# Performance work log

Measured on AMD Instinct MI355X. Metric: run time of the kernel, lower is better.

The kernel has to match this reference:

```python
import jax, jax.numpy as jnp
import numpy as np
from jax import lax

B, T, IN, D, K = 32, 4096, 12, 256, 1024
DECAY = 0.99
EPS_BN = 1e-5
EPS_VQ = 1e-5


def conv1d(x, w, b, pad):
    # x: (B, C, T), w: (O, I, k)
    y = lax.conv_general_dilated(x, w, window_strides=(1,), padding=[(pad, pad)],
                                 dimension_numbers=("NCH", "OIH", "NCH"))
    return y + b[None, :, None]


def batchnorm(x, g, be):
    # training-mode BatchNorm1d: stats over (B, T) per channel, biased variance
    m = jnp.mean(x, axis=(0, 2), keepdims=True)
    v = jnp.mean((x - m) ** 2, axis=(0, 2), keepdims=True)
    return (x - m) * lax.rsqrt(v + EPS_BN) * g[None, :, None] + be[None, :, None]


def setup_inputs() -> dict:
    key = jax.random.key(0)
    ks = jax.random.split(key, 16)
    inp = {"x": jax.random.normal(ks[0], (B, T, IN), dtype=jnp.float32)}
    fan_in = [IN] + [D] * 5
    for i in range(6):
        std = 1.0 / np.sqrt(fan_in[i] * 4)
        inp[f"w{i+1}"] = jax.random.normal(ks[1 + i], (D, fan_in[i], 4), dtype=jnp.float32) * std
        inp[f"b{i+1}"] = jnp.zeros((D,), dtype=jnp.float32)
    for i in range(5):
        inp[f"g{i+1}"] = jnp.ones((D,), dtype=jnp.float32)
        inp[f"be{i+1}"] = jnp.zeros((D,), dtype=jnp.float32)
    inp["codebook"] = jax.random.normal(ks[8], (K, D), dtype=jnp.float32)
    inp["ema_w"] = jax.random.normal(ks[9], (K, D), dtype=jnp.float32)
    inp["ema_cluster_size"] = jnp.zeros((K,), dtype=jnp.float32)
    return inp


def reference(x, w1, b1, g1, be1, w2, b2, g2, be2, w3, b3, g3, be3,
              w4, b4, g4, be4, w5, b5, g5, be5, w6, b6,
              codebook, ema_w, ema_cluster_size):
    h = jnp.transpose(x, (0, 2, 1))  # (B, IN, T)
    h = jax.nn.relu(batchnorm(conv1d(h, w1, b1, 2), g1, be1))
    h = jax.nn.relu(batchnorm(conv1d(h, w2, b2, 1), g2, be2))
    h = jax.nn.relu(batchnorm(conv1d(h, w3, b3, 2), g3, be3))
    h = jax.nn.relu(batchnorm(conv1d(h, w4, b4, 1), g4, be4))
    h = jax.nn.relu(batchnorm(conv1d(h, w5, b5, 2), g5, be5))
    h = conv1d(h, w6, b6, 1)
    z_e = jnp.transpose(h, (0, 2, 1))  # (B, T, D)

    # cdist(p=2) + argmin; sqrt is monotone so argmin over squared dist is identical
    d2 = (jnp.sum(z_e ** 2, axis=-1, keepdims=True)
          - 2.0 * jnp.einsum("btd,kd->btk", z_e, codebook)
          + jnp.sum(codebook ** 2, axis=-1))  # (B, T, K)
    ids = jnp.argmin(d2, axis=-1)  # (B, T)
    z_q = codebook[ids]  # (B, T, D)

    ids_flat = ids.reshape(-1)
    z_e_flat = z_e.reshape(-1, D)
    # one-hot.T @ z_e == segment_sum; one-hot column sums == counts
    n_i = jax.ops.segment_sum(jnp.ones_like(ids_flat, dtype=z_e.dtype), ids_flat, num_segments=K)
    sum_current = jax.ops.segment_sum(z_e_flat, ids_flat, num_segments=K)  # (K, D)

    new_ecs = ema_cluster_size * DECAY + (1.0 - DECAY) * n_i
    n = jnp.sum(new_ecs)
    smoothed = (new_ecs + EPS_VQ) / (n + K * EPS_VQ) * n
    new_ema_w = ema_w * DECAY + (1.0 - DECAY) * sum_current
    new_codebook = new_ema_w / smoothed[:, None]

    z_q_st = z_e + lax.stop_gradient(z_q - z_e)  # straight-through
    return z_e, z_q_st, new_codebook, new_ecs
```

## Files before the change

### kernel.cpp

```cpp
#include <hip/hip_runtime.h>
#include <cstdint>
#include <cstddef>


typedef _Float16 half8 __attribute__((ext_vector_type(8)));
typedef float f32x4 __attribute__((ext_vector_type(4)));

#define MFMA16(a, b, c) __builtin_amdgcn_mfma_f32_16x16x32_f16((a), (b), (c), 0, 0, 0)
#define INV2048 4.8828125e-4f

__device__ __forceinline__ void splitf(float v, _Float16& h, _Float16& l)
{
    _Float16 hh = (_Float16)v;
    h = hh;
    l = (_Float16)((v - (float)hh) * 2048.0f);
}
__device__ __forceinline__ float joinf(_Float16 h, _Float16 l)
{
    return (float)h + (float)l * INV2048;
}

__global__ __launch_bounds__(256)
void conv1_kernel(const float* __restrict__ x, const float* __restrict__ w1,
                  const float* __restrict__ b1, _Float16* __restrict__ YH,
                  _Float16* __restrict__ YL)
{
    const int b  = blockIdx.y;
    const int t0 = blockIdx.x * 32;
    const int oc = threadIdx.x;
    __shared__ float xl[35 * 12];
    for (int idx = threadIdx.x; idx < 420; idx += 256) {
        int tt = t0 - 2 + idx / 12;
        int i  = idx % 12;
        xl[idx] = (tt >= 0 && tt < 4096) ? x[((size_t)b * 4096 + tt) * 12 + i] : 0.f;
    }
    float w[48];
#pragma unroll
    for (int q = 0; q < 12; q++)
        *(float4*)&w[q * 4] = *(const float4*)(w1 + (size_t)oc * 48 + q * 4);
    __syncthreads();
    const float bias = b1[oc];
    for (int dt = 0; dt < 32; dt++) {
        int t = t0 + dt;
        if (t >= 4097) break;
        float a = bias;
#pragma unroll
        for (int i = 0; i < 12; i++)
#pragma unroll
            for (int k = 0; k < 4; k++)
                a = fmaf(xl[(dt + k) * 12 + i], w[i * 4 + k], a);
        _Float16 h, l;
        splitf(a, h, l);
        const size_t o = ((size_t)b * 4097 + t) * 256 + oc;
        YH[o] = h;
        YL[o] = l;
    }
}

__global__ __launch_bounds__(256)
void bn_partial_h(const _Float16* __restrict__ YH, const _Float16* __restrict__ YL,
                  int M, float* __restrict__ part)
{
    const int j = blockIdx.x;
    const int c = threadIdx.x;
    const int chunk = (M + 255) / 256;
    int r0 = j * chunk;
    int r1 = r0 + chunk; if (r1 > M) r1 = M;
    float s = 0.f, s2 = 0.f;
    for (int r = r0; r < r1; r++) {
        const size_t o = ((size_t)r << 8) + c;
        float v = joinf(YH[o], YL[o]);
        s += v;
        s2 = fmaf(v, v, s2);
    }
    part[j * 256 + c]         = s;
    part[65536 + j * 256 + c] = s2;
}

__global__ __launch_bounds__(256)
void bn_finalize(const float* __restrict__ part, const float* __restrict__ g,
                 const float* __restrict__ be, float invM, float* __restrict__ scsh)
{
    const int c = threadIdx.x;
    float s = 0.f, s2 = 0.f;
    for (int j = 0; j < 256; j++) {
        s  += part[j * 256 + c];
        s2 += part[65536 + j * 256 + c];
    }
    float mean = s * invM;
    float var  = fmaf(s2, invM, -mean * mean);
    float sc   = g[c] * rsqrtf(var + 1e-5f);
    scsh[c]       = sc;
    scsh[256 + c] = fmaf(-mean, sc, be[c]);
}

__global__ __launch_bounds__(256)
void bn_split_h(_Float16* __restrict__ YH, _Float16* __restrict__ YL,
                const float* __restrict__ scsh, int N8)
{
    int idx = blockIdx.x * 256 + threadIdx.x;
    const int stride = gridDim.x * 256;
    for (; idx < N8; idx += stride) {
        const size_t e0 = (size_t)idx * 8;
        const int ci0 = (int)(e0 & 255);
        half8 h = *(half8*)(YH + e0);
        half8 l = *(half8*)(YL + e0);
        float4 scA = *(const float4*)(scsh + ci0);
        float4 scB = *(const float4*)(scsh + ci0 + 4);
        float4 shA = *(const float4*)(scsh + 256 + ci0);
        float4 shB = *(const float4*)(scsh + 256 + ci0 + 4);
        float sc[8] = {scA.x, scA.y, scA.z, scA.w, scB.x, scB.y, scB.z, scB.w};
        float sh[8] = {shA.x, shA.y, shA.z, shA.w, shB.x, shB.y, shB.z, shB.w};
#pragma unroll
        for (int e = 0; e < 8; e++) {
            float v = joinf(h[e], l[e]);
            v = fmaxf(fmaf(v, sc[e], sh[e]), 0.f);
            _Float16 hh, ll;
            splitf(v, hh, ll);
            h[e] = hh;
            l[e] = ll;
        }
        *(half8*)(YH + e0) = h;
        *(half8*)(YL + e0) = l;
    }
}

__global__ __launch_bounds__(256)
void split8(const float* __restrict__ Z, _Float16* __restrict__ ZH,
            _Float16* __restrict__ ZL, int N8)
{
    int idx = blockIdx.x * 256 + threadIdx.x;
    const int stride = gridDim.x * 256;
    for (; idx < N8; idx += stride) {
        const size_t e0 = (size_t)idx * 8;
        float4 a = *(const float4*)(Z + e0);
        float4 b = *(const float4*)(Z + e0 + 4);
        float v[8] = {a.x, a.y, a.z, a.w, b.x, b.y, b.z, b.w};
        half8 h, l;
#pragma unroll
        for (int e = 0; e < 8; e++) {
            _Float16 hh, ll;
            splitf(v[e], hh, ll);
            h[e] = hh;
            l[e] = ll;
        }
        *(half8*)(ZH + e0) = h;
        *(half8*)(ZL + e0) = l;
    }
}

__global__ __launch_bounds__(256)
void prep_w_split(const float* __restrict__ w, _Float16* __restrict__ hi,
                  _Float16* __restrict__ lo)
{
    int idx = blockIdx.x * 256 + threadIdx.x;
    int o   = idx >> 10, rem = idx & 1023;
    int tap = rem >> 8,  ci  = rem & 255;
    float v = w[((size_t)o << 10) + (ci << 2) + tap];
    _Float16 h, l;
    splitf(v, h, l);
    hi[idx] = h;
    lo[idx] = l;
}

__global__ __launch_bounds__(256)
void prep_cnorm(const float* __restrict__ cb, float* __restrict__ cnorm)
{
    const int k = blockIdx.x;
    const int d = threadIdx.x;
    float v = cb[((size_t)k << 8) + d];
    __shared__ float sm[256];
    sm[d] = v * v;
    __syncthreads();
    for (int off = 128; off > 0; off >>= 1) {
        if (d < off) sm[d] += sm[d + off];
        __syncthreads();
    }
    if (d == 0) cnorm[k] = sm[0];
}

template<int T_IN, int T_OUT, int PAD, bool F32OUT>
__global__ __launch_bounds__(256)
void conv_gemm_mfma(const _Float16* __restrict__ XH, const _Float16* __restrict__ XL,
                    const _Float16* __restrict__ WH, const _Float16* __restrict__ WL,
                    const float* __restrict__ bias, float* __restrict__ Yf,
                    _Float16* __restrict__ YH, _Float16* __restrict__ YL)
{
    constexpr int M = 32 * T_OUT;
    __shared__ _Float16 AsH[4096], AsL[4096], BsH[4096], BsL[4096];

    const int tid  = threadIdx.x;
    const int lane = tid & 63;
    const int wv   = tid >> 6;
    const int fr   = lane & 15;
    const int kgf  = lane >> 4;
    const int m0 = blockIdx.y * 128;
    const int n0 = blockIdx.x * 128;

    const int haBase = wv * 1024 + ((fr * 32 + kgf * 8) ^ ((fr & 7) << 3));
    const int hbBase = (fr * 32 + kgf * 8) ^ ((fr & 7) << 3);

    const int skg = tid & 3;
    int wOff[2], tOut[2];
    long long aBase[2];
    size_t bBase[2];
    bool mok[2];
#pragma unroll
    for (int u = 0; u < 2; u++) {
        int r = (tid >> 2) + 64 * u;
        wOff[u] = (r * 32 + skg * 8) ^ ((r & 7) << 3);
        int m = m0 + r;
        mok[u] = (m < M);
        int b;
        if (T_OUT == 4096) b = m >> 12;
        else               b = (m - (m >> 12)) >> 12;
        int t = m - b * T_OUT;
        tOut[u]  = t;
        aBase[u] = (((long long)b * T_IN + t) << 8) + (skg << 3);
        bBase[u] = (((size_t)(n0 + r)) << 10) + (skg << 3);
    }

    half8 rAH[2], rAL[2], rBH[2], rBL[2];
    const half8 hz = {(_Float16)0, (_Float16)0, (_Float16)0, (_Float16)0,
                      (_Float16)0, (_Float16)0, (_Float16)0, (_Float16)0};

    auto LOAD = [&](int s) {
        const int tap = s >> 3;
        const int ci0 = (s & 7) << 5;
        const int dt  = tap - PAD;
#pragma unroll
        for (int u = 0; u < 2; u++) {
            const int ti = tOut[u] + dt;
            if (mok[u] && ti >= 0 && ti < T_IN) {
                const long long ga = aBase[u] + ((long long)dt << 8) + ci0;
                rAH[u] = *(const half8*)(XH + ga);
                rAL[u] = *(const half8*)(XL + ga);
            } else {
                rAH[u] = hz;
                rAL[u] = hz;
            }
            const size_t gb = bBase[u] + ((size_t)s << 5);
            rBH[u] = *(const half8*)(WH + gb);
            rBL[u] = *(const half8*)(WL + gb);
        }
    };

    f32x4 acc1[2][8], acc2[2][8];
#pragma unroll
    for (int i = 0; i < 2; i++)
#pragma unroll
        for (int j = 0; j < 8; j++) {
            acc1[i][j] = (f32x4){0.f, 0.f, 0.f, 0.f};
            acc2[i][j] = (f32x4){0.f, 0.f, 0.f, 0.f};
        }

    LOAD(0);
    for (int s = 0; s < 32; s++) {
        *(half8*)&AsH[wOff[0]] = rAH[0];
        *(half8*)&AsH[wOff[1]] = rAH[1];
        *(half8*)&AsL[wOff[0]] = rAL[0];
        *(half8*)&AsL[wOff[1]] = rAL[1];
        *(half8*)&BsH[wOff[0]] = rBH[0];
        *(half8*)&BsH[wOff[1]] = rBH[1];
        *(half8*)&BsL[wOff[0]] = rBL[0];
        *(half8*)&BsL[wOff[1]] = rBL[1];
        __syncthreads();
        if (s + 1 < 32) LOAD(s + 1);
        half8 ah0 = *(const half8*)&AsH[haBase];
        half8 ah1 = *(const half8*)&AsH[haBase + 512];
        half8 al0 = *(const half8*)&AsL[haBase];
        half8 al1 = *(const half8*)&AsL[haBase + 512];
#pragma unroll
        for (int j = 0; j < 8; j++) {
            half8 bh = *(const half8*)&BsH[hbBase + j * 512];
            half8 bl = *(const half8*)&BsL[hbBase + j * 512];
            acc1[0][j] = MFMA16(ah0, bh, acc1[0][j]);
            acc2[0][j] = MFMA16(ah0, bl, acc2[0][j]);
            acc2[0][j] = MFMA16(al0, bh, acc2[0][j]);
            acc1[1][j] = MFMA16(ah1, bh, acc1[1][j]);
            acc2[1][j] = MFMA16(ah1, bl, acc2[1][j]);
            acc2[1][j] = MFMA16(al1, bh, acc2[1][j]);
        }
        __syncthreads();
    }

    float bj[8];
#pragma unroll
    for (int j = 0; j < 8; j++) bj[j] = bias[n0 + j * 16 + fr];
#pragma unroll
    for (int i = 0; i < 2; i++)
#pragma unroll
        for (int q = 0; q < 4; q++) {
            const int m = m0 + wv * 32 + i * 16 + kgf * 4 + q;
            if (m < M) {
#pragma unroll
                for (int j = 0; j < 8; j++) {
                    float vv = acc1[i][j][q] + acc2[i][j][q] * INV2048 + bj[j];
                    const size_t o = ((size_t)m << 8) + n0 + j * 16 + fr;
                    if constexpr (F32OUT) {
                        Yf[o] = vv;
                    } else {
                        _Float16 h, l;
                        splitf(vv, h, l);
                        YH[o] = h;
                        YL[o] = l;
                    }
                }
            }
        }
}

__global__ __launch_bounds__(256)
void vq_argmin_mfma(const _Float16* __restrict__ ZH, const _Float16* __restrict__ ZL,
                    const _Float16* __restrict__ CH, const _Float16* __restrict__ CL,
                    const float* __restrict__ cnorm, int* __restrict__ ids)
{
    __shared__ _Float16 AsH[4096], AsL[4096], BsH[4096], BsL[4096];

    const int tid  = threadIdx.x;
    const int lane = tid & 63;
    const int wv   = tid >> 6;
    const int fr   = lane & 15;
    const int kgf  = lane >> 4;
    const int m0 = blockIdx.x * 128;

    const int haBase = wv * 1024 + ((fr * 32 + kgf * 8) ^ ((fr & 7) << 3));
    const int hbBase = (fr * 32 + kgf * 8) ^ ((fr & 7) << 3);

    const int skg = tid & 3;
    int wOff[2];
    size_t aBase[2], bBase[2];
#pragma unroll
    for (int u = 0; u < 2; u++) {
        int r = (tid >> 2) + 64 * u;
        wOff[u]  = (r * 32 + skg * 8) ^ ((r & 7) << 3);
        aBase[u] = (((size_t)(m0 + r)) << 8) + (skg << 3);
        bBase[u] = (((size_t)r) << 8) + (skg << 3);
    }

    half8 rAH[2], rAL[2], rBH[2], rBL[2];

    auto LOADV = [&](int ss) {
        const int nt = ss >> 3;
        const int dd = (ss & 7) << 5;
#pragma unroll
        for (int u = 0; u < 2; u++) {
            const size_t ga = aBase[u] + dd;
            rAH[u] = *(const half8*)(ZH + ga);
            rAL[u] = *(const half8*)(ZL + ga);
            const size_t gb = bBase[u] + ((size_t)nt << 15) + dd;
            rBH[u] = *(const half8*)(CH + gb);
            rBL[u] = *(const half8*)(CL + gb);
        }
    };

    float bv[2][4];
    int   bk[2][4];
#pragma unroll
    for (int i = 0; i < 2; i++)
#pragma unroll
        for (int q = 0; q < 4; q++) { bv[i][q] = 3.4e38f; bk[i][q] = 0; }

    f32x4 acc1[2][8], acc2[2][8];

    LOADV(0);
    for (int nt = 0; nt < 8; nt++) {
#pragma unroll
        for (int i = 0; i < 2; i++)
#pragma unroll
            for (int j = 0; j < 8; j++) {
                acc1[i][j] = (f32x4){0.f, 0.f, 0.f, 0.f};
                acc2[i][j] = (f32x4){0.f, 0.f, 0.f, 0.f};
            }
        for (int dstep = 0; dstep < 8; dstep++) {
            const int ss = nt * 8 + dstep;
            *(half8*)&AsH[wOff[0]] = rAH[0];
            *(half8*)&AsH[wOff[1]] = rAH[1];
            *(half8*)&AsL[wOff[0]] = rAL[0];
            *(half8*)&AsL[wOff[1]] = rAL[1];
            *(half8*)&BsH[wOff[0]] = rBH[0];
            *(half8*)&BsH[wOff[1]] = rBH[1];
            *(half8*)&BsL[wOff[0]] = rBL[0];
            *(half8*)&BsL[wOff[1]] = rBL[1];
            __syncthreads();
            if (ss + 1 < 64) LOADV(ss + 1);
            half8 ah0 = *(const half8*)&AsH[haBase];
            half8 ah1 = *(const half8*)&AsH[haBase + 512];
            half8 al0 = *(const half8*)&AsL[haBase];
            half8 al1 = *(const half8*)&AsL[haBase + 512];
#pragma unroll
            for (int j = 0; j < 8; j++) {
                half8 bh = *(const half8*)&BsH[hbBase + j * 512];
                half8 bl = *(const half8*)&BsL[hbBase + j * 512];
                acc1[0][j] = MFMA16(ah0, bh, acc1[0][j]);
                acc2[0][j] = MFMA16(ah0, bl, acc2[0][j]);
                acc2[0][j] = MFMA16(al0, bh, acc2[0][j]);
                acc1[1][j] = MFMA16(ah1, bh, acc1[1][j]);
                acc2[1][j] = MFMA16(ah1, bl, acc2[1][j]);
                acc2[1][j] = MFMA16(al1, bh, acc2[1][j]);
            }
            __syncthreads();
        }
        const int n0t = nt * 128;
#pragma unroll
        for (int j = 0; j < 8; j++) {
            const int code = n0t + j * 16 + fr;
            const float cn = cnorm[code];
#pragma unroll
            for (int i = 0; i < 2; i++)
#pragma unroll
                for (int q = 0; q < 4; q++) {
                    float s = fmaf(-2.f, acc1[i][j][q] + acc2[i][j][q] * INV2048, cn);
                    if (s < bv[i][q] || (s == bv[i][q] && code < bk[i][q])) {
                        bv[i][q] = s; bk[i][q] = code;
                    }
                }
        }
    }

#pragma unroll
    for (int i = 0; i < 2; i++)
#pragma unroll
        for (int q = 0; q < 4; q++) {
            float v = bv[i][q];
            int   k = bk[i][q];
            for (int msk = 1; msk < 16; msk <<= 1) {
                float ov = __shfl_xor(v, msk, 64);
                int   ok = __shfl_xor(k, msk, 64);
                if (ov < v || (ov == v && ok < k)) { v = ov; k = ok; }
            }
            if (fr == 0) ids[m0 + wv * 32 + i * 16 + kgf * 4 + q] = k;
        }
}

__global__ __launch_bounds__(256)
void vq_hist(const int* __restrict__ ids, unsigned* __restrict__ cnt)
{
    __shared__ unsigned lc[1024];
    const int t = threadIdx.x;
#pragma unroll
    for (int u = 0; u < 4; u++) lc[t + 256 * u] = 0u;
    __syncthreads();
    const int m = blockIdx.x * 256 + t;
    atomicAdd(&lc[ids[m]], 1u);
    __syncthreads();
#pragma unroll
    for (int u = 0; u < 4; u++) {
        const int c = t + 256 * u;
        const unsigned h = lc[c];
        if (h) atomicAdd(&cnt[c], h);
    }
}

__global__ __launch_bounds__(1024)
void vq_scan(const unsigned* __restrict__ cnt, int* __restrict__ offs, int* __restrict__ curs)
{
    __shared__ int sm[1024];
    const int k = threadIdx.x;
    const int c = (int)cnt[k];
    sm[k] = c;
    __syncthreads();
    for (int off = 1; off < 1024; off <<= 1) {
        int v = (k >= off) ? sm[k - off] : 0;
        __syncthreads();
        sm[k] += v;
        __syncthreads();
    }
    int exc = sm[k] - c;
    offs[k] = exc;
    curs[k] = exc;
    if (k == 1023) offs[1024] = sm[k];
}

__global__ __launch_bounds__(256)
void vq_scatter(const int* __restrict__ ids, int* __restrict__ curs,
                int* __restrict__ perm, int* __restrict__ scode)
{
    __shared__ int lcnt[1024];
    __shared__ int lbase[1024];
    const int t = threadIdx.x;
#pragma unroll
    for (int u = 0; u < 4; u++) lcnt[t + 256 * u] = 0;
    __syncthreads();
    const int m = blockIdx.x * 256 + t;
    const int id = ids[m];
    const int lrank = atomicAdd(&lcnt[id], 1);
    __syncthreads();
#pragma unroll
    for (int u = 0; u < 4; u++) {
        const int c = t + 256 * u;
        const int h = lcnt[c];
        if (h) lbase[c] = atomicAdd(&curs[c], h);
    }
    __syncthreads();
    const int pos = lbase[id] + lrank;
    perm[pos]  = m;
    scode[pos] = id;
}

__global__ __launch_bounds__(256)
void vq_gather_zq(const int* __restrict__ ids, const float* __restrict__ cb,
                  float* __restrict__ zq)
{
    const int row = blockIdx.x * 4 + (threadIdx.x >> 6);
    const int d4  = (threadIdx.x & 63) << 2;
    const int id  = ids[row];
    *(float4*)(zq + ((size_t)row << 8) + d4) =
        *(const float4*)(cb + ((size_t)id << 8) + d4);
}

__global__ __launch_bounds__(256)
void vq_segsum(const int* __restrict__ perm, const int* __restrict__ scode,
               const float* __restrict__ Z, float* __restrict__ sums)
{
    __shared__ int pm[256];
    __shared__ int cd[256];
    const int p0 = blockIdx.x * 256;
    const int d  = threadIdx.x;
    pm[d] = perm[p0 + d];
    cd[d] = scode[p0 + d];
    __syncthreads();
    float s = 0.f;
    int cur = cd[0];
    for (int i = 0; i < 256; i++) {
        int c = cd[i];
        float v = Z[((size_t)pm[i] << 8) + d];
        if (c != cur) {
            atomicAdd(&sums[((size_t)cur << 8) + d], s);
            s = 0.f;
            cur = c;
        }
        s += v;
    }
    atomicAdd(&sums[((size_t)cur << 8) + d], s);
}

__global__ __launch_bounds__(1024)
void vq_fin1(const unsigned* __restrict__ cnt, const float* __restrict__ ema_cs,
             float* __restrict__ ecs, float* __restrict__ nval)
{
    __shared__ float sm[1024];
    const int k = threadIdx.x;
    float e = fmaf(ema_cs[k], 0.99f, 0.01f * (float)cnt[k]);
    ecs[k] = e;
    sm[k] = e;
    __syncthreads();
    for (int off = 512; off > 0; off >>= 1) {
        if (k < off) sm[k] += sm[k + off];
        __syncthreads();
    }
    if (k == 0) nval[0] = sm[0];
}

__global__ __launch_bounds__(256)
void vq_fin2(const float* __restrict__ ema_w, const float* __restrict__ sums,
             const float* __restrict__ ecs, const float* __restrict__ nval,
             float* __restrict__ cbout)
{
    const int k = blockIdx.x, d = threadIdx.x;
    const float n = nval[0];
    const float sm = ((ecs[k] + 1e-5f) / (n + 0.01024f)) * n;
    const size_t idx = ((size_t)k << 8) + d;
    cbout[idx] = fmaf(ema_w[idx], 0.99f, 0.01f * sums[idx]) / sm;
}

extern "C" void kernel_launch(void* const* d_in, const int* in_sizes, int n_in,
                              void* d_out, int out_size, void* d_ws, size_t ws_size,
                              hipStream_t stream)
{
    (void)in_sizes; (void)n_in; (void)out_size; (void)ws_size;

    const float* x = (const float*)d_in[0];
    const float* w[7]; const float* bias[7];
    for (int i = 1; i <= 6; i++) {
        w[i]    = (const float*)d_in[1 + 2 * (i - 1)];
        bias[i] = (const float*)d_in[2 + 2 * (i - 1)];
    }
    const float* g[6]; const float* be[6];
    for (int i = 1; i <= 5; i++) {
        g[i]  = (const float*)d_in[13 + 2 * (i - 1)];
        be[i] = (const float*)d_in[14 + 2 * (i - 1)];
    }
    const float* codebook = (const float*)d_in[23];
    const float* ema_w    = (const float*)d_in[24];
    const float* ema_cs   = (const float*)d_in[25];

    float* out   = (float*)d_out;
    float* z_e   = out;
    float* z_q   = out + 33554432;
    float* cbout = out + 67108864;
    float* ecs   = out + 67371008;

    float* ws = (float*)d_ws;
    _Float16* pingH = (_Float16*)ws;
    _Float16* pingL = pingH + 33562624;
    _Float16* pongH = (_Float16*)z_q;
    _Float16* pongL = pongH + 33554432;

    float* wsf   = ws + 33562624;
    _Float16* wthi = (_Float16*)wsf;
    _Float16* wtlo = (_Float16*)(wsf + 655360);
    _Float16* cbhi = (_Float16*)(wsf + 1310720);
    _Float16* cblo = (_Float16*)(wsf + 1441792);
    float* cnorm = wsf + 1572864;
    float* scsh  = cnorm + 1024;
    float* part  = scsh + 2560;
    float* sums  = part + 131072;
    float* nval  = sums + 262144;
    int*      ids  = (int*)(nval + 16);
    unsigned* cnt  = (unsigned*)(ids + 131072);
    int*      offs = (int*)(cnt + 1024);
    int*      curs = offs + 1025;
    int*      perm = curs + 1024;
    int*      scode = (int*)part;

    hipMemsetAsync(cnt, 0, 1024 * sizeof(unsigned), stream);
    hipMemsetAsync(sums, 0, 262144 * sizeof(float), stream);

    for (int i = 0; i < 5; i++)
        prep_w_split<<<1024, 256, 0, stream>>>(w[i + 2], wthi + (size_t)i * 262144,
                                               wtlo + (size_t)i * 262144);
    split8<<<128, 256, 0, stream>>>(codebook, cbhi, cblo, 32768);
    prep_cnorm<<<1024, 256, 0, stream>>>(codebook, cnorm);

    conv1_kernel<<<dim3(129, 32), 256, 0, stream>>>(x, w[1], bias[1], pingH, pingL);
    bn_partial_h<<<256, 256, 0, stream>>>(pingH, pingL, 131104, part);
    bn_finalize<<<1, 256, 0, stream>>>(part, g[1], be[1], 1.f / 131104.f, scsh);
    bn_split_h<<<4096, 256, 0, stream>>>(pingH, pingL, scsh, 131104 * 32);

    conv_gemm_mfma<4097, 4096, 1, false><<<dim3(2, 1024), 256, 0, stream>>>(
        pingH, pingL, wthi, wtlo, bias[2], nullptr, pongH, pongL);
    bn_partial_h<<<256, 256, 0, stream>>>(pongH, pongL, 131072, part);
    bn_finalize<<<1, 256, 0, stream>>>(part, g[2], be[2], 1.f / 131072.f, scsh + 512);
    bn_split_h<<<4096, 256, 0, stream>>>(pongH, pongL, scsh + 512, 131072 * 32);

    conv_gemm_mfma<4096, 4097, 2, false><<<dim3(2, 1025), 256, 0, stream>>>(
        pongH, pongL, wthi + 262144, wtlo + 262144, bias[3], nullptr, pingH, pingL);
    bn_partial_h<<<256, 256, 0, stream>>>(pingH, pingL, 131104, part);
    bn_finalize<<<1, 256, 0, stream>>>(part, g[3], be[3], 1.f / 131104.f, scsh + 1024);
    bn_split_h<<<4096, 256, 0, stream>>>(pingH, pingL, scsh + 1024, 131104 * 32);

    conv_gemm_mfma<4097, 4096, 1, false><<<dim3(2, 1024), 256, 0, stream>>>(
        pingH, pingL, wthi + 524288, wtlo + 524288, bias[4], nullptr, pongH, pongL);
    bn_partial_h<<<256, 256, 0, stream>>>(pongH, pongL, 131072, part);
    bn_finalize<<<1, 256, 0, stream>>>(part, g[4], be[4], 1.f / 131072.f, scsh + 1536);
    bn_split_h<<<4096, 256, 0, stream>>>(pongH, pongL, scsh + 1536, 131072 * 32);

    conv_gemm_mfma<4096, 4097, 2, false><<<dim3(2, 1025), 256, 0, stream>>>(
        pongH, pongL, wthi + 786432, wtlo + 786432, bias[5], nullptr, pingH, pingL);
    bn_partial_h<<<256, 256, 0, stream>>>(pingH, pingL, 131104, part);
    bn_finalize<<<1, 256, 0, stream>>>(part, g[5], be[5], 1.f / 131104.f, scsh + 2048);
    bn_split_h<<<4096, 256, 0, stream>>>(pingH, pingL, scsh + 2048, 131104 * 32);

    conv_gemm_mfma<4097, 4096, 1, true><<<dim3(2, 1024), 256, 0, stream>>>(
        pingH, pingL, wthi + 1048576, wtlo + 1048576, bias[6], z_e, nullptr, nullptr);

    split8<<<4096, 256, 0, stream>>>(z_e, pongH, pongL, 4194304);
    vq_argmin_mfma<<<1024, 256, 0, stream>>>(pongH, pongL, cbhi, cblo, cnorm, ids);
    vq_hist<<<512, 256, 0, stream>>>(ids, cnt);
    vq_scan<<<1, 1024, 0, stream>>>(cnt, offs, curs);
    vq_scatter<<<512, 256, 0, stream>>>(ids, curs, perm, scode);
    vq_gather_zq<<<32768, 256, 0, stream>>>(ids, codebook, z_q);
    vq_segsum<<<512, 256, 0, stream>>>(perm, scode, z_e, sums);
    vq_fin1<<<1, 1024, 0, stream>>>(cnt, ema_cs, ecs, nval);
    vq_fin2<<<1024, 256, 0, stream>>>(ema_w, sums, ecs, nval, cbout);
}
```

Before: 3.203 ms.

## Fuse BN stats into conv GEMM epilogue and restructure MFMA tiles with double-buffered weights

Conv GEMM and VQ argmin kernels switch to a 2x2 wave tiling. A fragments now load straight from global into registers, while the B tile is double-buffered in LDS with one barrier per step and launch bounds set for two blocks per CU. The conv epilogue now accumulates per-channel sum and sum of squares through LDS and global atomics, which removes the separate bn_partial pass over each activation buffer. This trades an extra full read of each layer output for float atomics, which are non-deterministic, and reading A directly from global may cost more memory traffic.

```diff
diff --git a/kernel.cpp b/kernel.cpp
--- a/kernel.cpp
+++ b/kernel.cpp
@@ -87,6 +87,20 @@
         s  += part[j * 256 + c];
         s2 += part[65536 + j * 256 + c];
     }
+    float mean = s * invM;
+    float var  = fmaf(s2, invM, -mean * mean);
+    float sc   = g[c] * rsqrtf(var + 1e-5f);
+    scsh[c]       = sc;
+    scsh[256 + c] = fmaf(-mean, sc, be[c]);
+}
+
+__global__ __launch_bounds__(256)
+void bn_finalize2(const float* __restrict__ part2, const float* __restrict__ g,
+                  const float* __restrict__ be, float invM, float* __restrict__ scsh)
+{
+    const int c = threadIdx.x;
+    float s  = part2[c];
+    float s2 = part2[256 + c];
     float mean = s * invM;
     float var  = fmaf(s2, invM, -mean * mean);
     float sc   = g[c] * rsqrtf(var + 1e-5f);
@@ -179,124 +193,146 @@
     if (d == 0) cnorm[k] = sm[0];
 }
 
-template<int T_IN, int T_OUT, int PAD, bool F32OUT>
-__global__ __launch_bounds__(256)
+template<int T_IN, int T_OUT, int PAD, bool STATS, bool F32OUT>
+__global__ __launch_bounds__(256, 2)
 void conv_gemm_mfma(const _Float16* __restrict__ XH, const _Float16* __restrict__ XL,
                     const _Float16* __restrict__ WH, const _Float16* __restrict__ WL,
                     const float* __restrict__ bias, float* __restrict__ Yf,
-                    _Float16* __restrict__ YH, _Float16* __restrict__ YL)
+                    _Float16* __restrict__ YH, _Float16* __restrict__ YL,
+                    float* __restrict__ part2)
 {
     constexpr int M = 32 * T_OUT;
-    __shared__ _Float16 AsH[4096], AsL[4096], BsH[4096], BsL[4096];
+    __shared__ _Float16 BsH[2][4096], BsL[2][4096];
+    __shared__ float chS[128], chS2[128];
 
     const int tid  = threadIdx.x;
     const int lane = tid & 63;
     const int wv   = tid >> 6;
-    const int fr   = lane & 15;
-    const int kgf  = lane >> 4;
+    const int wr   = wv >> 1, wc = wv & 1;
+    const int fr   = lane & 15, kgf = lane >> 4;
     const int m0 = blockIdx.y * 128;
     const int n0 = blockIdx.x * 128;
 
-    const int haBase = wv * 1024 + ((fr * 32 + kgf * 8) ^ ((fr & 7) << 3));
-    const int hbBase = (fr * 32 + kgf * 8) ^ ((fr & 7) << 3);
-
-    const int skg = tid & 3;
-    int wOff[2], tOut[2];
-    long long aBase[2];
-    size_t bBase[2];
-    bool mok[2];
-#pragma unroll
-    for (int u = 0; u < 2; u++) {
-        int r = (tid >> 2) + 64 * u;
-        wOff[u] = (r * 32 + skg * 8) ^ ((r & 7) << 3);
-        int m = m0 + r;
-        mok[u] = (m < M);
+    const int rB   = tid >> 1;
+    const int su0  = (tid & 1) << 4;
+    const int swzB = (rB & 7) << 3;
+    const int bD0  = (rB * 32 + su0) ^ swzB;
+    const int bD1  = (rB * 32 + su0 + 8) ^ swzB;
+    const size_t bSrcRow = ((size_t)(n0 + rB)) << 10;
+
+    const int hbB = ((wc * 64 + fr) * 32 + kgf * 8) ^ ((fr & 7) << 3);
+
+    long long aAddr[4]; int tG[4]; bool mOK[4];
+#pragma unroll
+    for (int g = 0; g < 4; g++) {
+        int row = m0 + wr * 64 + g * 16 + fr;
+        bool ok = row < M;
+        int rr = ok ? row : 0;
         int b;
-        if (T_OUT == 4096) b = m >> 12;
-        else               b = (m - (m >> 12)) >> 12;
-        int t = m - b * T_OUT;
-        tOut[u]  = t;
-        aBase[u] = (((long long)b * T_IN + t) << 8) + (skg << 3);
-        bBase[u] = (((size_t)(n0 + r)) << 10) + (skg << 3);
-    }
-
-    half8 rAH[2], rAL[2], rBH[2], rBL[2];
+        if (T_OUT == 4096) b = rr >> 12;
+        else               b = (rr - (rr >> 12)) >> 12;
+        int t = rr - b * T_OUT;
+        mOK[g] = ok; tG[g] = t;
+        aAddr[g] = (((long long)b * T_IN + t) << 8) + kgf * 8;
+    }
+
     const half8 hz = {(_Float16)0, (_Float16)0, (_Float16)0, (_Float16)0,
                       (_Float16)0, (_Float16)0, (_Float16)0, (_Float16)0};
 
-    auto LOAD = [&](int s) {
+    f32x4 acc1[4][4], acc2[4][4];
+#pragma unroll
+    for (int g = 0; g < 4; g++)
+#pragma unroll
+        for (int j = 0; j < 4; j++) {
+            acc1[g][j] = (f32x4){0.f, 0.f, 0.f, 0.f};
+            acc2[g][j] = (f32x4){0.f, 0.f, 0.f, 0.f};
+        }
+
+    half8 a0H[4], a0L[4], a1H[4], a1L[4];
+
+    auto loadA = [&](int s, half8* dH, half8* dL) {
         const int tap = s >> 3;
         const int ci0 = (s & 7) << 5;
         const int dt  = tap - PAD;
 #pragma unroll
-        for (int u = 0; u < 2; u++) {
-            const int ti = tOut[u] + dt;
-            if (mok[u] && ti >= 0 && ti < T_IN) {
-                const long long ga = aBase[u] + ((long long)dt << 8) + ci0;
-                rAH[u] = *(const half8*)(XH + ga);
-                rAL[u] = *(const half8*)(XL + ga);
+        for (int g = 0; g < 4; g++) {
+            const int ti = tG[g] + dt;
+            if (mOK[g] && ti >= 0 && ti < T_IN) {
+                const long long ga = aAddr[g] + ((long long)dt << 8) + ci0;
+                dH[g] = *(const half8*)(XH + ga);
+                dL[g] = *(const half8*)(XL + ga);
             } else {
-                rAH[u] = hz;
-                rAL[u] = hz;
+                dH[g] = hz;
+                dL[g] = hz;
             }
-            const size_t gb = bBase[u] + ((size_t)s << 5);
-            rBH[u] = *(const half8*)(WH + gb);
-            rBL[u] = *(const half8*)(WL + gb);
         }
     };
 
-    f32x4 acc1[2][8], acc2[2][8];
-#pragma unroll
-    for (int i = 0; i < 2; i++)
-#pragma unroll
-        for (int j = 0; j < 8; j++) {
-            acc1[i][j] = (f32x4){0.f, 0.f, 0.f, 0.f};
-            acc2[i][j] = (f32x4){0.f, 0.f, 0.f, 0.f};
-        }
-
-    LOAD(0);
-    for (int s = 0; s < 32; s++) {
-        *(half8*)&AsH[wOff[0]] = rAH[0];
-        *(half8*)&AsH[wOff[1]] = rAH[1];
-        *(half8*)&AsL[wOff[0]] = rAL[0];
-        *(half8*)&AsL[wOff[1]] = rAL[1];
-        *(half8*)&BsH[wOff[0]] = rBH[0];
-        *(half8*)&BsH[wOff[1]] = rBH[1];
-        *(half8*)&BsL[wOff[0]] = rBL[0];
-        *(half8*)&BsL[wOff[1]] = rBL[1];
+    auto body = [&](int s, half8* aUH, half8* aUL, half8* aNH, half8* aNL) {
+        const int cur = s & 1;
+        const bool more = (s < 31);
+        half8 bRH0, bRH1, bRL0, bRL1;
+        if (more) {
+            const size_t gb = bSrcRow + (size_t)(s + 1) * 32 + su0;
+            bRH0 = *(const half8*)(WH + gb);
+            bRH1 = *(const half8*)(WH + gb + 8);
+            bRL0 = *(const half8*)(WL + gb);
+            bRL1 = *(const half8*)(WL + gb + 8);
+            loadA(s + 1, aNH, aNL);
+        }
+#pragma unroll
+        for (int j = 0; j < 4; j++) {
+            half8 bh = *(const half8*)&BsH[cur][hbB + j * 512];
+            half8 bl = *(const half8*)&BsL[cur][hbB + j * 512];
+#pragma unroll
+            for (int g = 0; g < 4; g++) {
+                acc1[g][j] = MFMA16(aUH[g], bh, acc1[g][j]);
+                acc2[g][j] = MFMA16(aUH[g], bl, acc2[g][j]);
+                acc2[g][j] = MFMA16(aUL[g], bh, acc2[g][j]);
+            }
+        }
+        if (more) {
+            *(half8*)&BsH[cur ^ 1][bD0] = bRH0;
+            *(half8*)&BsH[cur ^ 1][bD1] = bRH1;
+            *(half8*)&BsL[cur ^ 1][bD0] = bRL0;
+            *(half8*)&BsL[cur ^ 1][bD1] = bRL1;
+        }
         __syncthreads();
-        if (s + 1 < 32) LOAD(s + 1);
-        half8 ah0 = *(const half8*)&AsH[haBase];
-        half8 ah1 = *(const half8*)&AsH[haBase + 512];
-        half8 al0 = *(const half8*)&AsL[haBase];
-        half8 al1 = *(const half8*)&AsL[haBase + 512];
-#pragma unroll
-        for (int j = 0; j < 8; j++) {
-            half8 bh = *(const half8*)&BsH[hbBase + j * 512];
-            half8 bl = *(const half8*)&BsL[hbBase + j * 512];
-            acc1[0][j] = MFMA16(ah0, bh, acc1[0][j]);
-            acc2[0][j] = MFMA16(ah0, bl, acc2[0][j]);
-            acc2[0][j] = MFMA16(al0, bh, acc2[0][j]);
-            acc1[1][j] = MFMA16(ah1, bh, acc1[1][j]);
-            acc2[1][j] = MFMA16(ah1, bl, acc2[1][j]);
-            acc2[1][j] = MFMA16(al1, bh, acc2[1][j]);
-        }
+    };
+
+    {
+        const size_t gb = bSrcRow + su0;
+        *(half8*)&BsH[0][bD0] = *(const half8*)(WH + gb);
+        *(half8*)&BsH[0][bD1] = *(const half8*)(WH + gb + 8);
+        *(half8*)&BsL[0][bD0] = *(const half8*)(WL + gb);
+        *(half8*)&BsL[0][bD1] = *(const half8*)(WL + gb + 8);
+    }
+    loadA(0, a0H, a0L);
+    __syncthreads();
+
+    for (int sp = 0; sp < 32; sp += 2) {
+        body(sp,     a0H, a0L, a1H, a1L);
+        body(sp + 1, a1H, a1L, a0H, a0L);
+    }
+
+    if constexpr (STATS) {
+        if (tid < 128) { chS[tid] = 0.f; chS2[tid] = 0.f; }
         __syncthreads();
     }
-
-    float bj[8];
-#pragma unroll
-    for (int j = 0; j < 8; j++) bj[j] = bias[n0 + j * 16 + fr];
-#pragma unroll
-    for (int i = 0; i < 2; i++)
+    float bj[4];
+#pragma unroll
+    for (int j = 0; j < 4; j++) bj[j] = bias[n0 + wc * 64 + j * 16 + fr];
+    float js[4] = {0.f, 0.f, 0.f, 0.f}, js2[4] = {0.f, 0.f, 0.f, 0.f};
+#pragma unroll
+    for (int g = 0; g < 4; g++)
 #pragma unroll
         for (int q = 0; q < 4; q++) {
-            const int m = m0 + wv * 32 + i * 16 + kgf * 4 + q;
-            if (m < M) {
-#pragma unroll
-                for (int j = 0; j < 8; j++) {
-                    float vv = acc1[i][j][q] + acc2[i][j][q] * INV2048 + bj[j];
-                    const size_t o = ((size_t)m << 8) + n0 + j * 16 + fr;
+            const int row = m0 + wr * 64 + g * 16 + kgf * 4 + q;
+            if (row < M) {
+#pragma unroll
+                for (int j = 0; j < 4; j++) {
+                    float vv = acc1[g][j][q] + acc2[g][j][q] * INV2048 + bj[j];
+                    const size_t o = ((size_t)row << 8) + n0 + wc * 64 + j * 16 + fr;
                     if constexpr (F32OUT) {
                         Yf[o] = vv;
                     } else {
@@ -305,132 +341,172 @@
                         YH[o] = h;
                         YL[o] = l;
                     }
+                    if constexpr (STATS) {
+                        js[j] += vv;
+                        js2[j] = fmaf(vv, vv, js2[j]);
+                    }
                 }
             }
         }
-}
-
-__global__ __launch_bounds__(256)
+    if constexpr (STATS) {
+#pragma unroll
+        for (int j = 0; j < 4; j++) {
+            atomicAdd(&chS[wc * 64 + j * 16 + fr], js[j]);
+            atomicAdd(&chS2[wc * 64 + j * 16 + fr], js2[j]);
+        }
+        __syncthreads();
+        if (tid < 128) {
+            atomicAdd(&part2[n0 + tid], chS[tid]);
+            atomicAdd(&part2[256 + n0 + tid], chS2[tid]);
+        }
+    }
+}
+
+__global__ __launch_bounds__(256, 2)
 void vq_argmin_mfma(const _Float16* __restrict__ ZH, const _Float16* __restrict__ ZL,
                     const _Float16* __restrict__ CH, const _Float16* __restrict__ CL,
                     const float* __restrict__ cnorm, int* __restrict__ ids)
 {
-    __shared__ _Float16 AsH[4096], AsL[4096], BsH[4096], BsL[4096];
+    __shared__ _Float16 BsH[2][4096], BsL[2][4096];
+    __shared__ float rv[2][128];
+    __shared__ int   ri[2][128];
 
     const int tid  = threadIdx.x;
     const int lane = tid & 63;
     const int wv   = tid >> 6;
-    const int fr   = lane & 15;
-    const int kgf  = lane >> 4;
+    const int wr   = wv >> 1, wc = wv & 1;
+    const int fr   = lane & 15, kgf = lane >> 4;
     const int m0 = blockIdx.x * 128;
 
-    const int haBase = wv * 1024 + ((fr * 32 + kgf * 8) ^ ((fr & 7) << 3));
-    const int hbBase = (fr * 32 + kgf * 8) ^ ((fr & 7) << 3);
-
-    const int skg = tid & 3;
-    int wOff[2];
-    size_t aBase[2], bBase[2];
-#pragma unroll
-    for (int u = 0; u < 2; u++) {
-        int r = (tid >> 2) + 64 * u;
-        wOff[u]  = (r * 32 + skg * 8) ^ ((r & 7) << 3);
-        aBase[u] = (((size_t)(m0 + r)) << 8) + (skg << 3);
-        bBase[u] = (((size_t)r) << 8) + (skg << 3);
-    }
-
-    half8 rAH[2], rAL[2], rBH[2], rBL[2];
-
-    auto LOADV = [&](int ss) {
-        const int nt = ss >> 3;
-        const int dd = (ss & 7) << 5;
-#pragma unroll
-        for (int u = 0; u < 2; u++) {
-            const size_t ga = aBase[u] + dd;
-            rAH[u] = *(const half8*)(ZH + ga);
-            rAL[u] = *(const half8*)(ZL + ga);
-            const size_t gb = bBase[u] + ((size_t)nt << 15) + dd;
-            rBH[u] = *(const half8*)(CH + gb);
-            rBL[u] = *(const half8*)(CL + gb);
+    const int rB   = tid >> 1;
+    const int su0  = (tid & 1) << 4;
+    const int swzB = (rB & 7) << 3;
+    const int bD0  = (rB * 32 + su0) ^ swzB;
+    const int bD1  = (rB * 32 + su0 + 8) ^ swzB;
+
+    const int hbB = ((wc * 64 + fr) * 32 + kgf * 8) ^ ((fr & 7) << 3);
+
+    size_t aAddr[4];
+#pragma unroll
+    for (int g = 0; g < 4; g++)
+        aAddr[g] = (((size_t)(m0 + wr * 64 + g * 16 + fr)) << 8) + kgf * 8;
+
+    f32x4 acc1[4][4], acc2[4][4];
+    half8 a0H[4], a0L[4], a1H[4], a1L[4];
+
+    float bv[4][4];
+    int   bk[4][4];
+#pragma unroll
+    for (int g = 0; g < 4; g++)
+#pragma unroll
+        for (int q = 0; q < 4; q++) { bv[g][q] = 3.4e38f; bk[g][q] = 0; }
+
+    auto loadA = [&](int s, half8* dH, half8* dL) {
+        const int dd = (s & 7) << 5;
+#pragma unroll
+        for (int g = 0; g < 4; g++) {
+            const size_t ga = aAddr[g] + dd;
+            dH[g] = *(const half8*)(ZH + ga);
+            dL[g] = *(const half8*)(ZL + ga);
         }
     };
 
-    float bv[2][4];
-    int   bk[2][4];
-#pragma unroll
-    for (int i = 0; i < 2; i++)
-#pragma unroll
-        for (int q = 0; q < 4; q++) { bv[i][q] = 3.4e38f; bk[i][q] = 0; }
-
-    f32x4 acc1[2][8], acc2[2][8];
-
-    LOADV(0);
+    auto body = [&](int s, half8* aUH, half8* aUL, half8* aNH, half8* aNL) {
+        const int cur = s & 1;
+        const bool more = (s < 63);
+        half8 bRH0, bRH1, bRL0, bRL1;
+        if (more) {
+            const int s1 = s + 1;
+            const size_t gb = (((size_t)(((s1 >> 3) << 7) + rB)) << 8)
+                              + ((s1 & 7) << 5) + su0;
+            bRH0 = *(const half8*)(CH + gb);
+            bRH1 = *(const half8*)(CH + gb + 8);
+            bRL0 = *(const half8*)(CL + gb);
+            bRL1 = *(const half8*)(CL + gb + 8);
+            loadA(s1, aNH, aNL);
+        }
+#pragma unroll
+        for (int j = 0; j < 4; j++) {
+            half8 bh = *(const half8*)&BsH[cur][hbB + j * 512];
+            half8 bl = *(const half8*)&BsL[cur][hbB + j * 512];
+#pragma unroll
+            for (int g = 0; g < 4; g++) {
+                acc1[g][j] = MFMA16(aUH[g], bh, acc1[g][j]);
+                acc2[g][j] = MFMA16(aUH[g], bl, acc2[g][j]);
+                acc2[g][j] = MFMA16(aUL[g], bh, acc2[g][j]);
+            }
+        }
+        if (more) {
+            *(half8*)&BsH[cur ^ 1][bD0] = bRH0;
+            *(half8*)&BsH[cur ^ 1][bD1] = bRH1;
+            *(half8*)&BsL[cur ^ 1][bD0] = bRL0;
+            *(half8*)&BsL[cur ^ 1][bD1] = bRL1;
+        }
+        __syncthreads();
+    };
+
+    {
+        const size_t gb = (((size_t)rB) << 8) + su0;
+        *(half8*)&BsH[0][bD0] = *(const half8*)(CH + gb);
+        *(half8*)&BsH[0][bD1] = *(const half8*)(CH + gb + 8);
+        *(half8*)&BsL[0][bD0] = *(const half8*)(CL + gb);
+        *(half8*)&BsL[0][bD1] = *(const half8*)(CL + gb + 8);
+    }
+    loadA(0, a0H, a0L);
+    __syncthreads();
+
     for (int nt = 0; nt < 8; nt++) {
 #pragma unroll
-        for (int i = 0; i < 2; i++)
-#pragma unroll
-            for (int j = 0; j < 8; j++) {
-                acc1[i][j] = (f32x4){0.f, 0.f, 0.f, 0.f};
-                acc2[i][j] = (f32x4){0.f, 0.f, 0.f, 0.f};
+        for (int g = 0; g < 4; g++)
+#pragma unroll
+            for (int j = 0; j < 4; j++) {
+                acc1[g][j] = (f32x4){0.f, 0.f, 0.f, 0.f};
+                acc2[g][j] = (f32x4){0.f, 0.f, 0.f, 0.f};
             }
-        for (int dstep = 0; dstep < 8; dstep++) {
-            const int ss = nt * 8 + dstep;
-            *(half8*)&AsH[wOff[0]] = rAH[0];
-            *(half8*)&AsH[wOff[1]] = rAH[1];
-            *(half8*)&AsL[wOff[0]] = rAL[0];
-            *(half8*)&AsL[wOff[1]] = rAL[1];
-            *(half8*)&BsH[wOff[0]] = rBH[0];
-            *(half8*)&BsH[wOff[1]] = rBH[1];
-            *(half8*)&BsL[wOff[0]] = rBL[0];
-            *(half8*)&BsL[wOff[1]] = rBL[1];
-            __syncthreads();
-            if (ss + 1 < 64) LOADV(ss + 1);
-            half8 ah0 = *(const half8*)&AsH[haBase];
-            half8 ah1 = *(const half8*)&AsH[haBase + 512];
-            half8 al0 = *(const half8*)&AsL[haBase];
-            half8 al1 = *(const half8*)&AsL[haBase + 512];
-#pragma unroll
-            for (int j = 0; j < 8; j++) {
-                half8 bh = *(const half8*)&BsH[hbBase + j * 512];
-                half8 bl = *(const half8*)&BsL[hbBase + j * 512];
-                acc1[0][j] = MFMA16(ah0, bh, acc1[0][j]);
-                acc2[0][j] = MFMA16(ah0, bl, acc2[0][j]);
-                acc2[0][j] = MFMA16(al0, bh, acc2[0][j]);
-                acc1[1][j] = MFMA16(ah1, bh, acc1[1][j]);
-                acc2[1][j] = MFMA16(ah1, bl, acc2[1][j]);
-                acc2[1][j] = MFMA16(al1, bh, acc2[1][j]);
-            }
-            __syncthreads();
-        }
-        const int n0t = nt * 128;
-#pragma unroll
-        for (int j = 0; j < 8; j++) {
-            const int code = n0t + j * 16 + fr;
+        for (int sp = 0; sp < 8; sp += 2) {
+            const int s = nt * 8 + sp;
+            body(s,     a0H, a0L, a1H, a1L);
+            body(s + 1, a1H, a1L, a0H, a0L);
+        }
+#pragma unroll
+        for (int j = 0; j < 4; j++) {
+            const int code = nt * 128 + wc * 64 + j * 16 + fr;
             const float cn = cnorm[code];
 #pragma unroll
-            for (int i = 0; i < 2; i++)
+            for (int g = 0; g < 4; g++)
 #pragma unroll
                 for (int q = 0; q < 4; q++) {
-                    float s = fmaf(-2.f, acc1[i][j][q] + acc2[i][j][q] * INV2048, cn);
-                    if (s < bv[i][q] || (s == bv[i][q] && code < bk[i][q])) {
-                        bv[i][q] = s; bk[i][q] = code;
+                    float sscore = fmaf(-2.f, acc1[g][j][q] + acc2[g][j][q] * INV2048, cn);
+                    if (sscore < bv[g][q] || (sscore == bv[g][q] && code < bk[g][q])) {
+                        bv[g][q] = sscore; bk[g][q] = code;
                     }
                 }
         }
     }
 
 #pragma unroll
-    for (int i = 0; i < 2; i++)
+    for (int g = 0; g < 4; g++)
 #pragma unroll
         for (int q = 0; q < 4; q++) {
-            float v = bv[i][q];
-            int   k = bk[i][q];
+            float v = bv[g][q];
+            int   k = bk[g][q];
             for (int msk = 1; msk < 16; msk <<= 1) {
                 float ov = __shfl_xor(v, msk, 64);
                 int   ok = __shfl_xor(k, msk, 64);
                 if (ov < v || (ov == v && ok < k)) { v = ov; k = ok; }
             }
-            if (fr == 0) ids[m0 + wv * 32 + i * 16 + kgf * 4 + q] = k;
-        }
+            if (fr == 0) {
+                const int rloc = wr * 64 + g * 16 + kgf * 4 + q;
+                rv[wc][rloc] = v;
+                ri[wc][rloc] = k;
+            }
+        }
+    __syncthreads();
+    if (tid < 128) {
+        float v0 = rv[0][tid]; int k0 = ri[0][tid];
+        float v1 = rv[1][tid]; int k1 = ri[1][tid];
+        ids[m0 + tid] = (v1 < v0 || (v1 == v0 && k1 < k0)) ? k1 : k0;
+    }
 }
 
 __global__ __launch_bounds__(256)
@@ -613,9 +689,11 @@
     int*      curs = offs + 1025;
     int*      perm = curs + 1024;
     int*      scode = (int*)part;
+    float*    part2 = (float*)(perm + 131072);
 
     hipMemsetAsync(cnt, 0, 1024 * sizeof(unsigned), stream);
     hipMemsetAsync(sums, 0, 262144 * sizeof(float), stream);
+    hipMemsetAsync(part2, 0, 2048 * sizeof(float), stream);
 
     for (int i = 0; i < 5; i++)
         prep_w_split<<<1024, 256, 0, stream>>>(w[i + 2], wthi + (size_t)i * 262144,
@@ -628,32 +706,32 @@
     bn_finalize<<<1, 256, 0, stream>>>(part, g[1], be[1], 1.f / 131104.f, scsh);
     bn_split_h<<<4096, 256, 0, stream>>>(pingH, pingL, scsh, 131104 * 32);
 
-    conv_gemm_mfma<4097, 4096, 1, false><<<dim3(2, 1024), 256, 0, stream>>>(
-        pingH, pingL, wthi, wtlo, bias[2], nullptr, pongH, pongL);
-    bn_partial_h<<<256, 256, 0, stream>>>(pongH, pongL, 131072, part);
-    bn_finalize<<<1, 256, 0, stream>>>(part, g[2], be[2], 1.f / 131072.f, scsh + 512);
+    conv_gemm_mfma<4097, 4096, 1, true, false><<<dim3(2, 1024), 256, 0, stream>>>(
+        pingH, pingL, wthi, wtlo, bias[2], nullptr, pongH, pongL, part2);
+    bn_finalize2<<<1, 256, 0, stream>>>(part2, g[2], be[2], 1.f / 131072.f, scsh + 512);
     bn_split_h<<<4096, 256, 0, stream>>>(pongH, pongL, scsh + 512, 131072 * 32);
 
-    conv_gemm_mfma<4096, 4097, 2, false><<<dim3(2, 1025), 256, 0, stream>>>(
-        pongH, pongL, wthi + 262144, wtlo + 262144, bias[3], nullptr, pingH, pingL);
-    bn_partial_h<<<256, 256, 0, stream>>>(pingH, pingL, 131104, part);
-    bn_finalize<<<1, 256, 0, stream>>>(part, g[3], be[3], 1.f / 131104.f, scsh + 1024);
+    conv_gemm_mfma<4096, 4097, 2, true, false><<<dim3(2, 1025), 256, 0, stream>>>(
+        pongH, pongL, wthi + 262144, wtlo + 262144, bias[3], nullptr, pingH, pingL,
+        part2 + 512);
+    bn_finalize2<<<1, 256, 0, stream>>>(part2 + 512, g[3], be[3], 1.f / 131104.f, scsh + 1024);
     bn_split_h<<<4096, 256, 0, stream>>>(pingH, pingL, scsh + 1024, 131104 * 32);
 
-    conv_gemm_mfma<4097, 4096, 1, false><<<dim3(2, 1024), 256, 0, stream>>>(
-        pingH, pingL, wthi + 524288, wtlo + 524288, bias[4], nullptr, pongH, pongL);
-    bn_partial_h<<<256, 256, 0, stream>>>(pongH, pongL, 131072, part);
-    bn_finalize<<<1, 256, 0, stream>>>(part, g[4], be[4], 1.f / 131072.f, scsh + 1536);
+    conv_gemm_mfma<4097, 4096, 1, true, false><<<dim3(2, 1024), 256, 0, stream>>>(
+        pingH, pingL, wthi + 524288, wtlo + 524288, bias[4], nullptr, pongH, pongL,
+        part2 + 1024);
+    bn_finalize2<<<1, 256, 0, stream>>>(part2 + 1024, g[4], be[4], 1.f / 131072.f, scsh + 1536);
     bn_split_h<<<4096, 256, 0, stream>>>(pongH, pongL, scsh + 1536, 131072 * 32);
 
-    conv_gemm_mfma<4096, 4097, 2, false><<<dim3(2, 1025), 256, 0, stream>>>(
-        pongH, pongL, wthi + 786432, wtlo + 786432, bias[5], nullptr, pingH, pingL);
-    bn_partial_h<<<256, 256, 0, stream>>>(pingH, pingL, 131104, part);
-    bn_finalize<<<1, 256, 0, stream>>>(part, g[5], be[5], 1.f / 131104.f, scsh + 2048);
+    conv_gemm_mfma<4096, 4097, 2, true, false><<<dim3(2, 1025), 256, 0, stream>>>(
+        pongH, pongL, wthi + 786432, wtlo + 786432, bias[5], nullptr, pingH, pingL,
+        part2 + 1536);
+    bn_finalize2<<<1, 256, 0, stream>>>(part2 + 1536, g[5], be[5], 1.f / 131104.f, scsh + 2048);
     bn_split_h<<<4096, 256, 0, stream>>>(pingH, pingL, scsh + 2048, 131104 * 32);
 
-    conv_gemm_mfma<4097, 4096, 1, true><<<dim3(2, 1024), 256, 0, stream>>>(
-        pingH, pingL, wthi + 1048576, wtlo + 1048576, bias[6], z_e, nullptr, nullptr);
+    conv_gemm_mfma<4097, 4096, 1, false, true><<<dim3(2, 1024), 256, 0, stream>>>(
+        pingH, pingL, wthi + 1048576, wtlo + 1048576, bias[6], z_e, nullptr, nullptr,
+        nullptr);
 
     split8<<<4096, 256, 0, stream>>>(z_e, pongH, pongL, 4194304);
     vq_argmin_mfma<<<1024, 256, 0, stream>>>(pongH, pongL, cbhi, cblo, cnorm, ids);
```

Measured after the change: 3.192 ms. No clear change (-0.4%).
